# Kernel optimization log

Hardware: AMD Instinct MI355X
Metric: run time of the kernel (lower is better)

Reference implementation:

```python
import jax, jax.numpy as jnp
import numpy as np

B, N = 4, 8192
EPS = 1e-5

def _gather(points, idx):
    # points: (B, N, C); idx: (B, ...) int -> (B, ..., C)
    return jax.vmap(lambda p, i: p[i])(points, idx)

def _square_distance(src, dst):
    # src: (B,S,3), dst: (B,N,3) -> (B,S,N)
    return (jnp.sum(src * src, -1)[..., None]
            + jnp.sum(dst * dst, -1)[:, None, :]
            - 2.0 * jnp.einsum('bsc,bnc->bsn', src, dst))

def _fps(xyz, npoint):
    # farthest point sampling, deterministic start at index 0
    b, n, _ = xyz.shape
    def step(carry, _):
        distance, farthest = carry
        centroid = _gather(xyz, farthest)                # (B,3)
        d = jnp.sum((xyz - centroid[:, None, :]) ** 2, -1)
        distance = jnp.minimum(distance, d)
        return (distance, jnp.argmax(distance, -1).astype(jnp.int32)), farthest
    init = (jnp.full((b, n), 1e10, xyz.dtype), jnp.zeros((b,), jnp.int32))
    _, idx = jax.lax.scan(step, init, None, length=npoint)
    return jnp.transpose(idx)                            # (B, npoint)

def _query_ball(radius, nsample, xyz, new_xyz):
    n = xyz.shape[1]
    sqrdists = _square_distance(new_xyz, xyz)            # (B,S,N)
    gi = jnp.where(sqrdists > radius * radius, n, jnp.arange(n, dtype=jnp.int32))
    gi = jnp.sort(gi, axis=-1)[:, :, :nsample]           # (B,S,K)
    first = gi[:, :, :1]
    return jnp.where(gi == n, first, gi)

def _set_abstraction(xyz, points, npoint, radius, nsample, w, bconv, gamma, beta):
    fps_idx = _fps(xyz, npoint)
    new_xyz = _gather(xyz, fps_idx)                      # (B,S,3)
    idx = _query_ball(radius, nsample, xyz, new_xyz)     # (B,S,K)
    grouped = _gather(xyz, idx) - new_xyz[:, :, None, :] # (B,S,K,3) centered
    if points is not None:
        grouped = jnp.concatenate([grouped, _gather(points, idx)], -1)
    # shared MLP = 1x1 Conv2d + BatchNorm2d (training batch stats) + ReLU
    h = jnp.einsum('bskc,cd->bskd', grouped, w) + bconv
    mu = jnp.mean(h, axis=(0, 1, 2))
    var = jnp.var(h, axis=(0, 1, 2))
    h = jax.nn.relu((h - mu) * jax.lax.rsqrt(var + EPS) * gamma + beta)
    return new_xyz, jnp.max(h, axis=2)                   # max-pool over nsample

def setup_inputs():
    key = jax.random.key(0)
    ks = jax.random.split(key, 5)
    return {
        'xyz': jax.random.uniform(ks[0], (B, N, 6), jnp.float32),
        'w1': jax.random.normal(ks[1], (6, 128), jnp.float32) * 0.1,
        'b1': jax.random.normal(ks[2], (128,), jnp.float32) * 0.01,
        'g1': jnp.ones((128,), jnp.float32),
        'be1': jnp.zeros((128,), jnp.float32),
        'w2': jax.random.normal(ks[3], (131, 693), jnp.float32) * 0.05,
        'b2': jax.random.normal(ks[4], (693,), jnp.float32) * 0.01,
        'g2': jnp.ones((693,), jnp.float32),
        'be2': jnp.zeros((693,), jnp.float32),
    }

def reference(xyz, w1, b1, g1, be1, w2, b2, g2, be2):
    coords, norm = xyz[:, :, :3], xyz[:, :, 3:]
    l1_xyz, l1_pts = _set_abstraction(coords, norm, 2048, 0.0025, 32, w1, b1, g1, be1)
    l2_xyz, l2_pts = _set_abstraction(l1_xyz, l1_pts, 256, 0.005, 16, w2, b2, g2, be2)
    return l2_xyz, l2_pts  # (B,256,3), (B,256,693)
```

## Files before the change

### kernel.cpp

```cpp
#include <hip/hip_runtime.h>
#include <hip/hip_bf16.h>

__global__ void sentinel_k(float* out) {
  out[0] = 1000.0f;
}

__global__ __launch_bounds__(256) void zero_k(double* __restrict__ p, int n) {
  int i = blockIdx.x * 256 + threadIdx.x;
  if (i < n) p[i] = 0.0;
}

template<int PPT, int NPT, int NPTS, int STRIDE>
__global__ __launch_bounds__(512) void fps_k(const float* __restrict__ pts,
                                             float* __restrict__ out_xyz,
                                             float* __restrict__ out_f) {
  const int b = blockIdx.x, t = threadIdx.x;
  __shared__ unsigned long long warr[2][8];
  __shared__ float bc[2][3];
  float px[PPT], py[PPT], pz[PPT], dist[PPT];
  const int base = t * PPT;
  for (int j = 0; j < PPT; ++j) {
    const float* P = pts + (size_t)(b * NPTS + base + j) * STRIDE;
    px[j] = P[0]; py[j] = P[1]; pz[j] = P[2]; dist[j] = 1e10f;
  }
  if (t == 0) {
    bc[1][0] = px[0]; bc[1][1] = py[0]; bc[1][2] = pz[0];
    size_t o = (size_t)b * NPT * 3;
    out_xyz[o] = px[0]; out_xyz[o+1] = py[0]; out_xyz[o+2] = pz[0];
    if (out_f) { out_f[o] = px[0]; out_f[o+1] = py[0]; out_f[o+2] = pz[0]; }
  }
  __syncthreads();
  float cx = bc[1][0], cy = bc[1][1], cz = bc[1][2];
  const int lane = t & 63, wv = t >> 6;
  for (int s = 0; s < NPT - 1; ++s) {
    float vmax = -1.0f; int jb = 0;
    {
#pragma clang fp contract(off)
      for (int j = 0; j < PPT; ++j) {
        float dx = px[j] - cx, dy = py[j] - cy, dz = pz[j] - cz;
        float d = (dx*dx + dy*dy) + dz*dz;
        float dj = fminf(dist[j], d);
        dist[j] = dj;
        if (dj > vmax) { vmax = dj; jb = j; }
      }
    }
    unsigned long long key =
        ((unsigned long long)__float_as_uint(vmax) << 32) |
        (unsigned long long)(0xFFFFFFFFu - (unsigned)(base + jb));
    for (int off = 32; off; off >>= 1) {
      unsigned long long o = __shfl_down(key, off, 64);
      if (o > key) key = o;
    }
    const int p = s & 1;
    if (lane == 0) warr[p][wv] = key;
    __syncthreads();
    unsigned long long best = warr[p][0];
#pragma unroll
    for (int w = 1; w < 8; ++w) {
      unsigned long long k2 = warr[p][w];
      if (k2 > best) best = k2;
    }
    int ci = (int)(0xFFFFFFFFu - (unsigned)(best & 0xFFFFFFFFull));
    if (ci >= base && ci < base + PPT) {
      int j = ci - base;
      bc[p][0] = px[j]; bc[p][1] = py[j]; bc[p][2] = pz[j];
    }
    __syncthreads();
    cx = bc[p][0]; cy = bc[p][1]; cz = bc[p][2];
    if (t == 0) {
      size_t o = ((size_t)b * NPT + s + 1) * 3;
      out_xyz[o] = cx; out_xyz[o+1] = cy; out_xyz[o+2] = cz;
      if (out_f) { out_f[o] = cx; out_f[o+1] = cy; out_f[o+2] = cz; }
    }
  }
}

template<bool APPLY>
__global__ __launch_bounds__(256) void ball1_k(
    const float* __restrict__ xyz, const float* __restrict__ l1xyz,
    const float* __restrict__ w1, const float* __restrict__ b1,
    const double* __restrict__ A1, const double* __restrict__ B1,
    float* __restrict__ l1pts,
    double* __restrict__ S1R, double* __restrict__ S2R) {
  const int blk = blockIdx.x;
  const int b = blk >> 11, s = blk & 2047;
  const int t = threadIdx.x;
  __shared__ double w1s[768];
  __shared__ double b1s[128];
  __shared__ unsigned long long wm[4];
  __shared__ int lst[32];
  __shared__ double fls[32][6];
  __shared__ double red0[128], red1[128];

  for (int i = t; i < 768; i += 256) w1s[i] = (double)w1[i];
  if (t < 128) b1s[t] = (double)b1[t];

  const float* xb = xyz + (size_t)b * 8192 * 6;
  size_t co = ((size_t)b * 2048 + s) * 3;
  double cx = (double)l1xyz[co], cy = (double)l1xyz[co+1], cz = (double)l1xyz[co+2];

  const double R2 = 0.0025 * 0.0025;
  int cnt = 0;
  const int wvv = t >> 6, lane = t & 63;
  {
#pragma clang fp contract(off)
    double cs2 = (cx*cx + cy*cy) + cz*cz;
    for (int chunk = 0; chunk < 32 && cnt < 32; ++chunk) {
      int g = chunk * 256 + t;
      double x = (double)xb[(size_t)g*6];
      double y = (double)xb[(size_t)g*6+1];
      double z = (double)xb[(size_t)g*6+2];
      double pn2 = (x*x + y*y) + z*z;
      double dot = (cx*x + cy*y) + cz*z;
      double dsq = (cs2 + pn2) - 2.0 * dot;
      bool pred = !(dsq > R2);
      unsigned long long m = __ballot(pred);
      if (lane == 0) wm[wvv] = m;
      __syncthreads();
      int pre = 0, tot = 0;
      for (int w = 0; w < 4; ++w) {
        int c = __popcll(wm[w]);
        if (w < wvv) pre += c;
        tot += c;
      }
      if (pred) {
        int rank = cnt + pre + __popcll(m & ((1ull << lane) - 1ull));
        if (rank < 32) lst[rank] = g;
      }
      cnt += tot;
      __syncthreads();
    }
  }
  int cc = cnt < 32 ? cnt : 32;
  if (t >= cc && t < 32) lst[t] = lst[0];
  __syncthreads();
  if (t < 32) {
    int j = lst[t];
    fls[t][0] = (double)xb[(size_t)j*6]   - cx;
    fls[t][1] = (double)xb[(size_t)j*6+1] - cy;
    fls[t][2] = (double)xb[(size_t)j*6+2] - cz;
    fls[t][3] = (double)xb[(size_t)j*6+3];
    fls[t][4] = (double)xb[(size_t)j*6+4];
    fls[t][5] = (double)xb[(size_t)j*6+5];
  }
  __syncthreads();
  const int d = t & 127, kh = t >> 7;
  if (APPLY) {
    double a = A1[d], bb = B1[d];
    double vmax = -1e300;
    for (int k = kh; k < 32; k += 2) {
      double h = b1s[d];
#pragma unroll
      for (int c = 0; c < 6; ++c) h = fma(fls[k][c], w1s[c*128 + d], h);
      vmax = fmax(vmax, fma(a, h, bb));
    }
    if (kh == 1) red0[d] = vmax;
    __syncthreads();
    if (kh == 0) {
      double v = fmax(vmax, red0[d]);
      l1pts[((size_t)b * 2048 + s) * 128 + d] = (float)fmax(v, 0.0);
    }
  } else {
    double p1 = 0.0, p2 = 0.0;
    for (int k = kh; k < 32; k += 2) {
      double h = b1s[d];
#pragma unroll
      for (int c = 0; c < 6; ++c) h = fma(fls[k][c], w1s[c*128 + d], h);
      p1 += h; p2 = fma(h, h, p2);
    }
    if (kh == 1) { red0[d] = p1; red1[d] = p2; }
    __syncthreads();
    if (kh == 0) {
      int rep = blk & 7;
      atomicAdd(&S1R[(size_t)rep * 128 + d], p1 + red0[d]);
      atomicAdd(&S2R[(size_t)rep * 128 + d], p2 + red1[d]);
    }
  }
}

__global__ __launch_bounds__(256) void bn_finalize(const double* __restrict__ S1,
                                                   const double* __restrict__ S2,
                                                   int nrep, int D, double invN,
                                                   const float* __restrict__ g,
                                                   const float* __restrict__ be,
                                                   double* __restrict__ A, double* __restrict__ Bc) {
  int d = blockIdx.x * 256 + threadIdx.x;
  if (d >= D) return;
  double s1 = 0.0, s2 = 0.0;
  for (int r = 0; r < nrep; ++r) {
    s1 += S1[(size_t)r * D + d];
    s2 += S2[(size_t)r * D + d];
  }
  double mu = s1 * invN;
  double var = s2 * invN - mu * mu;
  double a = (double)g[d] / sqrt(var + 1e-5);
  A[d]  = a;
  Bc[d] = (double)be[d] - mu * a;
}

template<bool APPLY>
__global__ __launch_bounds__(256) void ball2_k(
    const float* __restrict__ l1xyz, const float* __restrict__ l1pts,
    const float* __restrict__ l2xyz,
    const float* __restrict__ w2, const float* __restrict__ b2,
    const double* __restrict__ A2, const double* __restrict__ B2,
    float* __restrict__ outp,
    double* __restrict__ T1R, double* __restrict__ T2R) {
  const int blk = blockIdx.x;
  const int b = blk >> 8, s = blk & 255;
  const int t = threadIdx.x;
  __shared__ double fT[131][16];
  __shared__ unsigned long long wm[4];
  __shared__ int lst[16];
  const float* Pb = l1xyz + (size_t)b * 2048 * 3;
  size_t co = ((size_t)b * 256 + s) * 3;
  double cx = (double)l2xyz[co], cy = (double)l2xyz[co+1], cz = (double)l2xyz[co+2];
  const double R2 = 0.005 * 0.005;
  int cnt = 0;
  const int wvv = t >> 6, lane = t & 63;
  {
#pragma clang fp contract(off)
    double cs2 = (cx*cx + cy*cy) + cz*cz;
    for (int chunk = 0; chunk < 8 && cnt < 16; ++chunk) {
      int g = chunk * 256 + t;
      double x = (double)Pb[(size_t)g*3];
      double y = (double)Pb[(size_t)g*3+1];
      double z = (double)Pb[(size_t)g*3+2];
      double pn2 = (x*x + y*y) + z*z;
      double dot = (cx*x + cy*y) + cz*z;
      double dsq = (cs2 + pn2) - 2.0 * dot;
      bool pred = !(dsq > R2);
      unsigned long long m = __ballot(pred);
      if (lane == 0) wm[wvv] = m;
      __syncthreads();
      int pre = 0, tot = 0;
      for (int w = 0; w < 4; ++w) {
        int c = __popcll(wm[w]);
        if (w < wvv) pre += c;
        tot += c;
      }
      if (pred) {
        int rank = cnt + pre + __popcll(m & ((1ull << lane) - 1ull));
        if (rank < 16) lst[rank] = g;
      }
      cnt += tot;
      __syncthreads();
    }
  }
  int cc = cnt < 16 ? cnt : 16;
  if (t >= cc && t < 16) lst[t] = lst[0];
  __syncthreads();
  for (int i = t; i < 16 * 131; i += 256) {
    int k = i & 15, c = i >> 4;
    int j = lst[k];
    double v;
    if (c == 0)      v = (double)Pb[(size_t)j*3]   - cx;
    else if (c == 1) v = (double)Pb[(size_t)j*3+1] - cy;
    else if (c == 2) v = (double)Pb[(size_t)j*3+2] - cz;
    else             v = (double)l1pts[((size_t)b*2048 + j)*128 + (c-3)];
    fT[c][k] = v;
  }
  __syncthreads();
  const int rep = blk & 7;
  for (int dd = 0; dd < 3; ++dd) {
    int d = t + dd * 256;
    if (d >= 693) break;
    double acc[16];
    double bv = (double)b2[d];
#pragma unroll
    for (int k = 0; k < 16; ++k) acc[k] = bv;
    for (int c = 0; c < 131; ++c) {
      double wv2 = (double)w2[(size_t)c * 693 + d];
#pragma unroll
      for (int k = 0; k < 16; ++k) acc[k] = fma(fT[c][k], wv2, acc[k]);
    }
    if (APPLY) {
      double a = A2[d], bb = B2[d];
      double vmax = -1e300;
#pragma unroll
      for (int k = 0; k < 16; ++k) vmax = fmax(vmax, fma(a, acc[k], bb));
      outp[((size_t)b * 256 + s) * 693 + d] = (float)fmax(vmax, 0.0);
    } else {
      double p1 = 0.0, p2 = 0.0;
#pragma unroll
      for (int k = 0; k < 16; ++k) { p1 += acc[k]; p2 = fma(acc[k], acc[k], p2); }
      atomicAdd(&T1R[(size_t)rep * 693 + d], p1);
      atomicAdd(&T2R[(size_t)rep * 693 + d], p2);
    }
  }
}

extern "C" void kernel_launch(void* const* d_in, const int* in_sizes, int n_in,
                              void* d_out, int out_size, void* d_ws, size_t ws_size,
                              hipStream_t stream) {
  (void)out_size;
  float* out = (float*)d_out;

  const int want[9] = {196608, 768, 128, 128, 128, 90783, 693, 693, 693};
  bool ok = (n_in == 9);
  for (int i = 0; ok && i < 9; ++i) ok = (in_sizes[i] == want[i]);
  const size_t REQ = 4600000;
  if (!ok || ws_size < REQ) {
    sentinel_k<<<1, 1, 0, stream>>>(out);
    return;
  }

  const float* xyz = (const float*)d_in[0];
  const float* w1  = (const float*)d_in[1];
  const float* b1  = (const float*)d_in[2];
  const float* g1  = (const float*)d_in[3];
  const float* be1 = (const float*)d_in[4];
  const float* w2  = (const float*)d_in[5];
  const float* b2  = (const float*)d_in[6];
  const float* g2  = (const float*)d_in[7];
  const float* be2 = (const float*)d_in[8];

  double* S1R = (double*)d_ws;
  double* S2R = S1R + 1024;
  double* T1R = S2R + 1024;
  double* T2R = T1R + 5544;
  double* A1  = T2R + 5544;
  double* B1  = A1 + 128;
  double* A2  = B1 + 128;
  double* B2  = A2 + 693;
  float* l1xyz = (float*)(B2 + 693);
  float* l2xyz = l1xyz + 24576;
  float* l1pts = l2xyz + 3072;

  zero_k<<<52, 256, 0, stream>>>(S1R, 13136);

  fps_k<16, 2048, 8192, 6><<<4, 512, 0, stream>>>(xyz, l1xyz, nullptr);
  fps_k<4, 256, 2048, 3><<<4, 512, 0, stream>>>(l1xyz, l2xyz, out);

  ball1_k<false><<<8192, 256, 0, stream>>>(xyz, l1xyz, w1, b1, nullptr, nullptr,
                                           nullptr, S1R, S2R);
  bn_finalize<<<1, 256, 0, stream>>>(S1R, S2R, 8, 128, 1.0 / (8192.0 * 32.0), g1, be1, A1, B1);
  ball1_k<true><<<8192, 256, 0, stream>>>(xyz, l1xyz, w1, b1, A1, B1,
                                          l1pts, S1R, S2R);

  ball2_k<false><<<1024, 256, 0, stream>>>(l1xyz, l1pts, l2xyz, w2, b2, nullptr, nullptr,
                                           nullptr, T1R, T2R);
  bn_finalize<<<3, 256, 0, stream>>>(T1R, T2R, 8, 693, 1.0 / (1024.0 * 16.0), g2, be2, A2, B2);
  ball2_k<true><<<1024, 256, 0, stream>>>(l1xyz, l1pts, l2xyz, w2, b2, A2, B2,
                                          out + 3072, T1R, T2R);
}
```

Measured before the change: 3.787 ms.

## Streamline FPS reduction with DPP wave max and per-wave centroid broadcast

```diff
diff --git a/kernel.cpp b/kernel.cpp
--- a/kernel.cpp
+++ b/kernel.cpp
@@ -1,5 +1,21 @@
 #include <hip/hip_runtime.h>
 #include <hip/hip_bf16.h>
+
+#define DEV __device__ __forceinline__
+
+DEV float wave_max_f32(float v) {
+#define STEPDPP(ctrl) { int iv = __float_as_int(v); \
+    int sh = __builtin_amdgcn_update_dpp(iv, iv, ctrl, 0xf, 0xf, false); \
+    v = fmaxf(v, __int_as_float(sh)); }
+  STEPDPP(0x111)
+  STEPDPP(0x112)
+  STEPDPP(0x114)
+  STEPDPP(0x118)
+  STEPDPP(0x142)
+  STEPDPP(0x143)
+#undef STEPDPP
+  return __int_as_float(__builtin_amdgcn_readlane(__float_as_int(v), 63));
+}
 
 __global__ void sentinel_k(float* out) {
   out[0] = 1000.0f;
@@ -15,8 +31,8 @@
                                              float* __restrict__ out_xyz,
                                              float* __restrict__ out_f) {
   const int b = blockIdx.x, t = threadIdx.x;
-  __shared__ unsigned long long warr[2][8];
-  __shared__ float bc[2][3];
+  __shared__ unsigned long long wkey[2][8];
+  __shared__ float wcx[2][8], wcy[2][8], wcz[2][8];
   float px[PPT], py[PPT], pz[PPT], dist[PPT];
   const int base = t * PPT;
   for (int j = 0; j < PPT; ++j) {
@@ -24,49 +40,57 @@
     px[j] = P[0]; py[j] = P[1]; pz[j] = P[2]; dist[j] = 1e10f;
   }
   if (t == 0) {
-    bc[1][0] = px[0]; bc[1][1] = py[0]; bc[1][2] = pz[0];
+    wcx[1][0] = px[0]; wcy[1][0] = py[0]; wcz[1][0] = pz[0];
     size_t o = (size_t)b * NPT * 3;
     out_xyz[o] = px[0]; out_xyz[o+1] = py[0]; out_xyz[o+2] = pz[0];
     if (out_f) { out_f[o] = px[0]; out_f[o+1] = py[0]; out_f[o+2] = pz[0]; }
   }
   __syncthreads();
-  float cx = bc[1][0], cy = bc[1][1], cz = bc[1][2];
+  float cx = wcx[1][0], cy = wcy[1][0], cz = wcz[1][0];
   const int lane = t & 63, wv = t >> 6;
   for (int s = 0; s < NPT - 1; ++s) {
-    float vmax = -1.0f; int jb = 0;
+    float vA = -1.0f, vB = -1.0f;
+    int jA = 0, jB = PPT / 2;
+    float axA = 0.f, ayA = 0.f, azA = 0.f, axB = 0.f, ayB = 0.f, azB = 0.f;
     {
 #pragma clang fp contract(off)
-      for (int j = 0; j < PPT; ++j) {
+      for (int j = 0; j < PPT / 2; ++j) {
         float dx = px[j] - cx, dy = py[j] - cy, dz = pz[j] - cz;
         float d = (dx*dx + dy*dy) + dz*dz;
         float dj = fminf(dist[j], d);
         dist[j] = dj;
-        if (dj > vmax) { vmax = dj; jb = j; }
-      }
-    }
-    unsigned long long key =
-        ((unsigned long long)__float_as_uint(vmax) << 32) |
-        (unsigned long long)(0xFFFFFFFFu - (unsigned)(base + jb));
-    for (int off = 32; off; off >>= 1) {
-      unsigned long long o = __shfl_down(key, off, 64);
-      if (o > key) key = o;
-    }
+        if (dj > vA) { vA = dj; jA = j; axA = px[j]; ayA = py[j]; azA = pz[j]; }
+      }
+      for (int j = PPT / 2; j < PPT; ++j) {
+        float dx = px[j] - cx, dy = py[j] - cy, dz = pz[j] - cz;
+        float d = (dx*dx + dy*dy) + dz*dz;
+        float dj = fminf(dist[j], d);
+        dist[j] = dj;
+        if (dj > vB) { vB = dj; jB = j; axB = px[j]; ayB = py[j]; azB = pz[j]; }
+      }
+    }
+    float vmax; int jb; float bx, by, bz;
+    if (vB > vA) { vmax = vB; jb = jB; bx = axB; by = ayB; bz = azB; }
+    else         { vmax = vA; jb = jA; bx = axA; by = ayA; bz = azA; }
+
+    float wmax = wave_max_f32(vmax);
+    unsigned long long mb = __ballot(vmax == wmax);
+    int wl = __ffsll((unsigned long long)mb) - 1;
     const int p = s & 1;
-    if (lane == 0) warr[p][wv] = key;
+    if (lane == wl) {
+      wkey[p][wv] = ((unsigned long long)__float_as_uint(wmax) << 32) |
+                    (unsigned long long)(0xFFFFFFFFu - (unsigned)(base + jb));
+      wcx[p][wv] = bx; wcy[p][wv] = by; wcz[p][wv] = bz;
+    }
     __syncthreads();
-    unsigned long long best = warr[p][0];
+    unsigned long long bestk = wkey[p][0];
+    int bw = 0;
 #pragma unroll
     for (int w = 1; w < 8; ++w) {
-      unsigned long long k2 = warr[p][w];
-      if (k2 > best) best = k2;
-    }
-    int ci = (int)(0xFFFFFFFFu - (unsigned)(best & 0xFFFFFFFFull));
-    if (ci >= base && ci < base + PPT) {
-      int j = ci - base;
-      bc[p][0] = px[j]; bc[p][1] = py[j]; bc[p][2] = pz[j];
-    }
-    __syncthreads();
-    cx = bc[p][0]; cy = bc[p][1]; cz = bc[p][2];
+      unsigned long long k2 = wkey[p][w];
+      if (k2 > bestk) { bestk = k2; bw = w; }
+    }
+    cx = wcx[p][bw]; cy = wcy[p][bw]; cz = wcz[p][bw];
     if (t == 0) {
       size_t o = ((size_t)b * NPT + s + 1) * 3;
       out_xyz[o] = cx; out_xyz[o+1] = cy; out_xyz[o+2] = cz;
```

Result: faster. 3.393 ms (-10.4%).
